# Kernel optimization log

Measured on AMD Instinct MI355X. Metric: run time of the kernel, lower is better.

Reference implementation:

```python
import jax, jax.numpy as jnp
import numpy as np

EPS = 1e-9

def setup_inputs() -> dict:
    key = jax.random.key(0)
    k1, k2, k3, k4 = jax.random.split(key, 4)
    B, D, M, R, C = 1024, 16, 4, 4096, 64
    x = jax.random.normal(k1, (B, D), dtype=jnp.float32)
    centers = jax.random.normal(k2, (D, M), dtype=jnp.float32)
    widths = jnp.ones((D, M), dtype=jnp.float32)
    consequents = jax.random.normal(k3, (R, D + 1, C), dtype=jnp.float32)
    rules = jax.random.randint(k4, (R, D), 0, M)  # rule -> MF index per input dim
    return {"x": x, "centers": centers, "widths": widths,
            "consequents": consequents, "rules": rules}

def reference(x, centers, widths, consequents, rules):
    B, D = x.shape
    # Gaussian membership values: [B, D, M]
    mfs = jnp.exp(-(x[:, :, None] - centers[None]) ** 2 / (2.0 * widths[None] ** 2)) + EPS
    # Gather per-rule MFs: rule_mfs[b, d, r] = mfs[b, d, rules[r, d]] -> [B, D, R]
    rule_mfs = jnp.take_along_axis(mfs, rules.T[None, :, :], axis=2)
    # Product firing strengths and normalization: [B, R]
    fs = jnp.prod(rule_mfs, axis=1)
    nfs = fs / (fs.sum(axis=1, keepdims=True) + EPS)
    # Extended input with bias: [B, D+1]
    x_ext = jnp.concatenate([x, jnp.ones((B, 1), dtype=x.dtype)], axis=1)
    # NOTE: faithful to the original torch code: 'bi,rjc->brc' has no shared
    # contraction index, so it sums x_ext over i and consequents over j.
    rule_out = jnp.einsum('br,brc->bc', nfs,
                          jnp.einsum('bi,rjc->brc', x_ext, consequents))
    return rule_out, nfs, x_ext
```

## Files before the change

kernel.cpp:

```cpp
#include <hip/hip_runtime.h>
#include <hip/hip_bf16.h>

typedef __attribute__((ext_vector_type(8))) short short8;
typedef __attribute__((ext_vector_type(4))) short short4v;
typedef __attribute__((ext_vector_type(4))) float floatx4;
typedef __attribute__((ext_vector_type(4))) unsigned int uintx4;
typedef unsigned int u32;
typedef unsigned short u16;

#define NB 1024
#define ND 16
#define NM 4
#define NR 4096
#define NC 64
#define EPSF 1e-9f
#define KSPLIT 16

__device__ inline u16 f2bf(float f) {
    u32 u;
    __builtin_memcpy(&u, &f, 4);
    u32 lsb = (u >> 16) & 1;
    u += 0x7fffu + lsb;
    return (u16)(u >> 16);
}

__global__ __launch_bounds__(256) void k_prep(const float* __restrict__ cons,
                                              const int* __restrict__ rules,
                                              u16* __restrict__ s_consT,
                                              u32* __restrict__ packed,
                                              float* __restrict__ out_rule) {
    __shared__ u16 tile[16][68];
    int rbase = blockIdx.x * 16;
    int tid = threadIdx.x;
    int c = tid & 63;
    out_rule[blockIdx.x * 256 + tid] = 0.f;
    {
        int rr = tid >> 6;
#pragma unroll
        for (int it = 0; it < 4; ++it, rr += 4) {
            const float* p = cons + (size_t)(rbase + rr) * (ND + 1) * NC + c;
            float s = 0.f;
#pragma unroll
            for (int j = 0; j < ND + 1; ++j) s += p[j * NC];
            tile[rr][c] = f2bf(s);
        }
    }
    if (tid < 16) {
        const int* q = rules + (size_t)(rbase + tid) * ND;
        u32 pk = 0;
#pragma unroll
        for (int d = 0; d < ND; ++d) pk |= ((u32)(q[d] & 3)) << (2 * d);
        packed[rbase + tid] = pk;
    }
    __syncthreads();
    {
        int cc = tid >> 2;
        int r0 = (tid & 3) * 4;
        short4v v;
#pragma unroll
        for (int e = 0; e < 4; ++e) v[e] = (short)tile[r0 + e][cc];
        *(short4v*)(s_consT + (size_t)cc * NR + rbase + r0) = v;
    }
}

__global__ __launch_bounds__(256) void k_fs(const float* __restrict__ x,
                                            const float* __restrict__ centers,
                                            const float* __restrict__ widths,
                                            const u32* __restrict__ packed,
                                            float* __restrict__ out_nfs,
                                            float* __restrict__ out_xe,
                                            float* __restrict__ sx) {
    __shared__ float xv[16];
    __shared__ float mftab[64];
    __shared__ float gtab[1024];
    __shared__ float wred[4];
    __shared__ float s_inv;
    int b = blockIdx.x;
    int tid = threadIdx.x;
    if (tid < 16) {
        float raw = x[b * 16 + tid];
        xv[tid] = raw;
        out_xe[b * 17 + tid] = raw;
    }
    if (tid == 16) out_xe[b * 17 + 16] = 1.0f;
    __syncthreads();
    if (tid < 64) {
        float diff = xv[tid >> 2] - centers[tid];
        float w = widths[tid];
        mftab[tid] = __expf(-diff * diff / (2.f * w * w)) + EPSF;
    }
    if (tid == 0) {
        float s = 1.f;
        for (int i = 0; i < 16; ++i) s += xv[i];
        sx[b] = s;
    }
    __syncthreads();
    for (int idx = tid; idx < 1024; idx += 256) {
        int g = idx >> 8, i = idx & 255;
        const float* mf = mftab + g * 16;
        gtab[idx] = mf[0 + (i & 3)] * mf[4 + ((i >> 2) & 3)] *
                    mf[8 + ((i >> 4) & 3)] * mf[12 + ((i >> 6) & 3)];
    }
    __syncthreads();
    floatx4 f[4];
    float lsum = 0.f;
#pragma unroll
    for (int it = 0; it < 4; ++it) {
        int r = it * 1024 + tid * 4;
        uintx4 p = *(const uintx4*)(packed + r);
#pragma unroll
        for (int e = 0; e < 4; ++e) {
            u32 pk = p[e];
            f[it][e] = gtab[pk & 255] * gtab[256 + ((pk >> 8) & 255)] *
                       gtab[512 + ((pk >> 16) & 255)] * gtab[768 + (pk >> 24)];
            lsum += f[it][e];
        }
    }
    for (int off = 32; off; off >>= 1) lsum += __shfl_down(lsum, off, 64);
    if ((tid & 63) == 0) wred[tid >> 6] = lsum;
    __syncthreads();
    if (tid == 0) s_inv = 1.f / (wred[0] + wred[1] + wred[2] + wred[3] + EPSF);
    __syncthreads();
    float inv = s_inv;
    float* on = out_nfs + (size_t)b * NR;
#pragma unroll
    for (int it = 0; it < 4; ++it) {
        int r = it * 1024 + tid * 4;
        floatx4 v;
#pragma unroll
        for (int e = 0; e < 4; ++e) v[e] = f[it][e] * inv;
        *(floatx4*)(on + r) = v;
    }
}

__global__ __launch_bounds__(256) void k_gemm(const float* __restrict__ nfs,
                                              const u16* __restrict__ s_consT,
                                              const float* __restrict__ sx,
                                              float* __restrict__ out_rule) {
    int rt = blockIdx.x;
    int ks = blockIdx.y;
    int tid = threadIdx.x;
    int wid = tid >> 6, lane = tid & 63;
    int arow = rt * 64 + wid * 16 + (lane & 15);
    int kbase = ks * (NR / KSPLIT) + (lane >> 4) * 8;
    const float* aptr = nfs + (size_t)arow * NR + kbase;
    const u16* bptr = s_consT + (size_t)(lane & 15) * NR + kbase;
    floatx4 acc[4] = {};
#pragma unroll
    for (int t = 0; t < (NR / KSPLIT) / 32; ++t) {
        floatx4 alo = *(const floatx4*)(aptr + t * 32);
        floatx4 ahi = *(const floatx4*)(aptr + t * 32 + 4);
        short8 af;
#pragma unroll
        for (int e = 0; e < 4; ++e) {
            af[e] = (short)f2bf(alo[e]);
            af[e + 4] = (short)f2bf(ahi[e]);
        }
#pragma unroll
        for (int cb = 0; cb < 4; ++cb) {
            short8 bf = *(const short8*)(bptr + (size_t)cb * 16 * NR + t * 32);
            acc[cb] = __builtin_amdgcn_mfma_f32_16x16x32_bf16(af, bf, acc[cb], 0, 0, 0);
        }
    }
    int orow0 = rt * 64 + wid * 16 + (lane >> 4) * 4;
    float s4[4];
#pragma unroll
    for (int reg = 0; reg < 4; ++reg) s4[reg] = sx[orow0 + reg];
#pragma unroll
    for (int cb = 0; cb < 4; ++cb)
#pragma unroll
        for (int reg = 0; reg < 4; ++reg) {
            int col = cb * 16 + (lane & 15);
            atomicAdd(out_rule + (size_t)(orow0 + reg) * NC + col, acc[cb][reg] * s4[reg]);
        }
}

extern "C" void kernel_launch(void* const* d_in, const int* in_sizes, int n_in,
                              void* d_out, int out_size, void* d_ws, size_t ws_size,
                              hipStream_t stream) {
    const float* x = (const float*)d_in[0];
    const float* centers = (const float*)d_in[1];
    const float* widths = (const float*)d_in[2];
    const float* cons = (const float*)d_in[3];
    const int* rules = (const int*)d_in[4];

    float* out = (float*)d_out;
    float* out_rule = out;
    float* out_nfs = out + NB * NC;
    float* out_xe = out + NB * NC + NB * NR;

    char* ws = (char*)d_ws;
    u16* s_consT = (u16*)ws;
    u32* packed = (u32*)(ws + (512 << 10));
    float* sx = (float*)(ws + (512 << 10) + (16 << 10));

    k_prep<<<NR / 16, 256, 0, stream>>>(cons, rules, s_consT, packed, out_rule);
    k_fs<<<NB, 256, 0, stream>>>(x, centers, widths, packed, out_nfs, out_xe, sx);
    k_gemm<<<dim3(16, KSPLIT), 256, 0, stream>>>(out_nfs, s_consT, sx, out_rule);
}
```

Measured before the change: 32.02 us.

## Overlap consequent prep with firing strengths; replace atomics with split-K partial reduction

Moves rule packing into a tiny dedicated kernel. Consequent summation/transposition now runs as extra blocks inside the firing-strength kernel, so the two independent stages overlap in a single launch. The GEMM no longer zeroes the output and uses float atomics. Each K-split block writes its partial tile to workspace, and the last-arriving block (tracked by an atomic counter) reduces all partials and applies the sx scaling. This adds partial-buffer traffic and a serialized final reduction per row tile, and it depends on correct fence/counter ordering.

```diff
diff --git a/kernel.cpp b/kernel.cpp
--- a/kernel.cpp
+++ b/kernel.cpp
@@ -5,6 +5,7 @@
 typedef __attribute__((ext_vector_type(4))) short short4v;
 typedef __attribute__((ext_vector_type(4))) float floatx4;
 typedef __attribute__((ext_vector_type(4))) unsigned int uintx4;
+typedef __attribute__((ext_vector_type(4))) int intx4;
 typedef unsigned int u32;
 typedef unsigned short u16;
 
@@ -24,59 +25,61 @@
     return (u16)(u >> 16);
 }
 
-__global__ __launch_bounds__(256) void k_prep(const float* __restrict__ cons,
-                                              const int* __restrict__ rules,
-                                              u16* __restrict__ s_consT,
-                                              u32* __restrict__ packed,
-                                              float* __restrict__ out_rule) {
+__global__ __launch_bounds__(256) void k_pack(const int* __restrict__ rules,
+                                              u32* __restrict__ packed) {
+    int r = blockIdx.x * 256 + threadIdx.x;
+    const int* q = rules + (size_t)r * ND;
+    u32 pk = 0;
+#pragma unroll
+    for (int i = 0; i < 4; ++i) {
+        intx4 v = *(const intx4*)(q + i * 4);
+#pragma unroll
+        for (int e = 0; e < 4; ++e) pk |= ((u32)(v[e] & 3)) << (2 * (i * 4 + e));
+    }
+    packed[r] = pk;
+}
+
+__global__ __launch_bounds__(256) void k_mid(const float* __restrict__ cons,
+                                             const float* __restrict__ x,
+                                             const float* __restrict__ centers,
+                                             const float* __restrict__ widths,
+                                             const u32* __restrict__ packed,
+                                             u16* __restrict__ s_consT,
+                                             float* __restrict__ out_nfs,
+                                             float* __restrict__ out_xe,
+                                             float* __restrict__ sx,
+                                             int* __restrict__ cnt) {
     __shared__ u16 tile[16][68];
-    int rbase = blockIdx.x * 16;
-    int tid = threadIdx.x;
-    int c = tid & 63;
-    out_rule[blockIdx.x * 256 + tid] = 0.f;
-    {
-        int rr = tid >> 6;
-#pragma unroll
-        for (int it = 0; it < 4; ++it, rr += 4) {
-            const float* p = cons + (size_t)(rbase + rr) * (ND + 1) * NC + c;
-            float s = 0.f;
-#pragma unroll
-            for (int j = 0; j < ND + 1; ++j) s += p[j * NC];
-            tile[rr][c] = f2bf(s);
-        }
-    }
-    if (tid < 16) {
-        const int* q = rules + (size_t)(rbase + tid) * ND;
-        u32 pk = 0;
-#pragma unroll
-        for (int d = 0; d < ND; ++d) pk |= ((u32)(q[d] & 3)) << (2 * d);
-        packed[rbase + tid] = pk;
-    }
-    __syncthreads();
-    {
-        int cc = tid >> 2;
-        int r0 = (tid & 3) * 4;
-        short4v v;
-#pragma unroll
-        for (int e = 0; e < 4; ++e) v[e] = (short)tile[r0 + e][cc];
-        *(short4v*)(s_consT + (size_t)cc * NR + rbase + r0) = v;
-    }
-}
-
-__global__ __launch_bounds__(256) void k_fs(const float* __restrict__ x,
-                                            const float* __restrict__ centers,
-                                            const float* __restrict__ widths,
-                                            const u32* __restrict__ packed,
-                                            float* __restrict__ out_nfs,
-                                            float* __restrict__ out_xe,
-                                            float* __restrict__ sx) {
     __shared__ float xv[16];
     __shared__ float mftab[64];
     __shared__ float gtab[1024];
     __shared__ float wred[4];
     __shared__ float s_inv;
-    int b = blockIdx.x;
+    int bid = blockIdx.x;
     int tid = threadIdx.x;
+    if (bid < 256) {
+        if (bid == 0 && tid < KSPLIT) cnt[tid] = 0;
+        int rbase = bid * 16;
+        int c = tid & 63;
+        int rr = tid >> 6;
+#pragma unroll
+        for (int it = 0; it < 4; ++it, rr += 4) {
+            const float* p = cons + (size_t)(rbase + rr) * (ND + 1) * NC + c;
+            float s = 0.f;
+#pragma unroll
+            for (int j = 0; j < ND + 1; ++j) s += p[j * NC];
+            tile[rr][c] = f2bf(s);
+        }
+        __syncthreads();
+        int cc = tid >> 2;
+        int r0 = (tid & 3) * 4;
+        short4v v;
+#pragma unroll
+        for (int e = 0; e < 4; ++e) v[e] = (short)tile[r0 + e][cc];
+        *(short4v*)(s_consT + (size_t)cc * NR + rbase + r0) = v;
+        return;
+    }
+    int b = bid - 256;
     if (tid < 16) {
         float raw = x[b * 16 + tid];
         xv[tid] = raw;
@@ -136,6 +139,8 @@
 __global__ __launch_bounds__(256) void k_gemm(const float* __restrict__ nfs,
                                               const u16* __restrict__ s_consT,
                                               const float* __restrict__ sx,
+                                              float* __restrict__ part,
+                                              int* __restrict__ cnt,
                                               float* __restrict__ out_rule) {
     int rt = blockIdx.x;
     int ks = blockIdx.y;
@@ -162,17 +167,33 @@
             acc[cb] = __builtin_amdgcn_mfma_f32_16x16x32_bf16(af, bf, acc[cb], 0, 0, 0);
         }
     }
-    int orow0 = rt * 64 + wid * 16 + (lane >> 4) * 4;
-    float s4[4];
-#pragma unroll
-    for (int reg = 0; reg < 4; ++reg) s4[reg] = sx[orow0 + reg];
+    float* po = part + ((size_t)rt * KSPLIT + ks) * (64 * 64);
+    int row0 = wid * 16 + (lane >> 4) * 4;
 #pragma unroll
     for (int cb = 0; cb < 4; ++cb)
 #pragma unroll
-        for (int reg = 0; reg < 4; ++reg) {
-            int col = cb * 16 + (lane & 15);
-            atomicAdd(out_rule + (size_t)(orow0 + reg) * NC + col, acc[cb][reg] * s4[reg]);
-        }
+        for (int reg = 0; reg < 4; ++reg)
+            po[(size_t)(row0 + reg) * 64 + cb * 16 + (lane & 15)] = acc[cb][reg];
+
+    __builtin_amdgcn_fence(__ATOMIC_RELEASE, "agent");
+    __syncthreads();
+    __shared__ int last;
+    if (tid == 0) {
+        int v = __hip_atomic_fetch_add(&cnt[rt], 1, __ATOMIC_ACQ_REL, __HIP_MEMORY_SCOPE_AGENT);
+        last = (v == KSPLIT - 1);
+    }
+    __syncthreads();
+    if (!last) return;
+    __builtin_amdgcn_fence(__ATOMIC_ACQUIRE, "agent");
+    const float* pr = part + (size_t)rt * KSPLIT * (64 * 64);
+#pragma unroll
+    for (int it = 0; it < 16; ++it) {
+        int o = it * 256 + tid;
+        float a = 0.f;
+#pragma unroll
+        for (int k2 = 0; k2 < KSPLIT; ++k2) a += pr[(size_t)k2 * (64 * 64) + o];
+        out_rule[(size_t)rt * 4096 + o] = a * sx[rt * 64 + (o >> 6)];
+    }
 }
 
 extern "C" void kernel_launch(void* const* d_in, const int* in_sizes, int n_in,
@@ -193,8 +214,11 @@
     u16* s_consT = (u16*)ws;
     u32* packed = (u32*)(ws + (512 << 10));
     float* sx = (float*)(ws + (512 << 10) + (16 << 10));
-
-    k_prep<<<NR / 16, 256, 0, stream>>>(cons, rules, s_consT, packed, out_rule);
-    k_fs<<<NB, 256, 0, stream>>>(x, centers, widths, packed, out_nfs, out_xe, sx);
-    k_gemm<<<dim3(16, KSPLIT), 256, 0, stream>>>(out_nfs, s_consT, sx, out_rule);
-}
+    int* cnt = (int*)(ws + (512 << 10) + (20 << 10));
+    float* part = (float*)(ws + (512 << 10) + (24 << 10));
+
+    k_pack<<<NR / 256, 256, 0, stream>>>(rules, packed);
+    k_mid<<<256 + NB, 256, 0, stream>>>(cons, x, centers, widths, packed,
+                                        s_consT, out_nfs, out_xe, sx, cnt);
+    k_gemm<<<dim3(16, KSPLIT), 256, 0, stream>>>(out_nfs, s_consT, sx, part, cnt, out_rule);
+}
```

Measured after the change: 60.67 us. 1.89x slower.
